# Kernel optimization log

Measured on AMD Instinct MI355X. Metric: run time of the kernel, lower is better.

Reference implementation:

```python
import jax, jax.numpy as jnp
import numpy as np

NUM_HEADS = 12
DIM = 768
NV = 4  # number of views
EPS = 1e-6


def _ln(x, g, b):
    m = x.mean(-1, keepdims=True)
    v = ((x - m) ** 2).mean(-1, keepdims=True)
    return (x - m) / jnp.sqrt(v + EPS) * g + b


def setup_inputs() -> dict:
    key = jax.random.key(0)
    ks = jax.random.split(key, 10)
    B, N, C, H = 4, 256, DIM, NUM_HEADS
    Hid = 4 * C
    s = 0.02
    return {
        'X': jax.random.normal(ks[0], (B * NV, N, C), jnp.float32),
        'norm1_g': jnp.ones((C,), jnp.float32),
        'norm1_b': jnp.zeros((C,), jnp.float32),
        'qkv_w': jax.random.normal(ks[1], (NV, 3 * C, C), jnp.float32) * s,
        'proj_w': jax.random.normal(ks[2], (NV, C, C), jnp.float32) * s,
        'proj_b': jnp.zeros((NV, C), jnp.float32),
        'norm2_g': jnp.ones((NV, C), jnp.float32),
        'norm2_b': jnp.zeros((NV, C), jnp.float32),
        'fc1_w': jax.random.normal(ks[3], (NV, Hid, C), jnp.float32) * s,
        'fc1_b': jnp.zeros((NV, Hid), jnp.float32),
        'fc2_w': jax.random.normal(ks[4], (NV, C, Hid), jnp.float32) * s,
        'fc2_b': jnp.zeros((NV, C), jnp.float32),
        'query': jax.random.normal(ks[5], (1, 1, C), jnp.float32),
        'mha_in_w': jax.random.normal(ks[6], (NV, 3 * C, C), jnp.float32) * s,
        'mha_in_b': jnp.zeros((NV, 3 * C), jnp.float32),
        'mha_out_w': jax.random.normal(ks[7], (NV, C, C), jnp.float32) * s,
        'mha_out_b': jnp.zeros((NV, C), jnp.float32),
    }


def reference(X, norm1_g, norm1_b, qkv_w, proj_w, proj_b, norm2_g, norm2_b,
              fc1_w, fc1_b, fc2_w, fc2_b, query, mha_in_w, mha_in_b,
              mha_out_w, mha_out_b):
    B4, N, C = X.shape
    B = B4 // NV
    H = NUM_HEADS
    hd = C // H
    scale = hd ** -0.5

    Xv = X.reshape(B, NV, N, C)
    Xn = _ln(Xv, norm1_g, norm1_b)

    # ---- FusionAttention: 4x4 pairwise cross attention between views ----
    qkv = jnp.einsum('bvnc,vdc->vbnd', Xn, qkv_w)              # [V,B,N,3C]
    qkv = qkv.reshape(NV, B, N, 3, H, hd).transpose(3, 0, 1, 4, 2, 5)  # [3,V,B,H,N,hd]
    q, k, v = qkv[0], qkv[1], qkv[2]
    scores = jnp.einsum('ibhnd,jbhmd->ijbhnm', q, k) * scale   # [V,V,B,H,N,N]
    attn = jax.nn.softmax(scores, axis=-1)
    ctx = jnp.einsum('ijbhnm,jbhmd->ijbhnd', attn, v)
    ctx = ctx.transpose(0, 1, 2, 4, 3, 5).reshape(NV, NV, B, N, C)
    # proj_i is affine, so mean over j of proj(x_j) == proj(mean_j x_j)
    ctx_mean = ctx.mean(axis=1)                                # [V,B,N,C]
    xa = jnp.einsum('vbnc,voc->vbno', ctx_mean, proj_w) + proj_b[:, None, None, :]

    x = xa * 2.0
    h = _ln(x, norm2_g[:, None, None, :], norm2_b[:, None, None, :])
    h1 = jax.nn.gelu(jnp.einsum('vbnc,vhc->vbnh', h, fc1_w) + fc1_b[:, None, None, :],
                     approximate=False)
    h2 = jnp.einsum('vbnh,vch->vbnc', h1, fc2_w) + fc2_b[:, None, None, :]
    x = x + h2                                                  # [V,B,N,C]

    # ---- CrossAttentionWithLearnableQuery (query identical for all T,B) ----
    wq, wk, wv = jnp.split(mha_in_w, 3, axis=1)                 # each [V,C,C]
    bq, bk, bv = jnp.split(mha_in_b, 3, axis=1)                 # each [V,C]
    q0 = query.reshape(C)
    qh = (jnp.einsum('c,vdc->vd', q0, wq) + bq).reshape(NV, H, hd)
    kh = (jnp.einsum('vbnc,vdc->vbnd', x, wk) + bk[:, None, None, :]).reshape(NV, B, N, H, hd)
    vh = (jnp.einsum('vbnc,vdc->vbnd', x, wv) + bv[:, None, None, :]).reshape(NV, B, N, H, hd)
    s2 = jnp.einsum('vhd,vbnhd->vbhn', qh, kh) * scale
    a2 = jax.nn.softmax(s2, axis=-1)
    c2 = jnp.einsum('vbhn,vbnhd->vbhd', a2, vh).reshape(NV, B, C)
    o = jnp.einsum('vbc,voc->vbo', c2, mha_out_w) + mha_out_b[:, None, :]  # [V,B,C]
    o = o.transpose(1, 0, 2).reshape(B, NV * C)                 # concat views
    # every query position produces identical output -> broadcast over T=N
    return jnp.broadcast_to(o[:, None, :], (B, N, NV * C))
```

## Files before the change

kernel.cpp:

```cpp
#include <hip/hip_runtime.h>
#include <math.h>

#define NVIEW 4
#define BATCH 4
#define NSEQ  256
#define CDIM  768
#define HEADS 12
#define HD    64

typedef __attribute__((ext_vector_type(8))) short   short8;
typedef __attribute__((ext_vector_type(8))) unsigned short ushort8;
typedef __attribute__((ext_vector_type(4))) float   float4v;

typedef const __attribute__((address_space(1))) void gas_t;
typedef       __attribute__((address_space(3))) void las_t;

__device__ __forceinline__ unsigned short f2b(float x)
{
    union { float f; unsigned u; } c; c.f = x;
    unsigned r = (c.u + 0x7FFFu + ((c.u >> 16) & 1u)) >> 16;
    return (unsigned short)r;
}

__global__ void conv_bf16(const float* __restrict__ src, unsigned short* __restrict__ dst, int n)
{
    int idx = (blockIdx.x * 256 + threadIdx.x) * 8;
    if (idx >= n) return;
    float4 a = *(const float4*)(src + idx);
    float4 b = *(const float4*)(src + idx + 4);
    ushort8 o;
    o[0] = f2b(a.x); o[1] = f2b(a.y); o[2] = f2b(a.z); o[3] = f2b(a.w);
    o[4] = f2b(b.x); o[5] = f2b(b.y); o[6] = f2b(b.z); o[7] = f2b(b.w);
    *(ushort8*)(dst + idx) = o;
}

__device__ __forceinline__ void block_ln_row_b(const float* __restrict__ xrow,
                                               const float* __restrict__ g,
                                               const float* __restrict__ b,
                                               unsigned short* __restrict__ orow)
{
    const int t = threadIdx.x;
    float x0 = xrow[t], x1 = xrow[t + 256], x2 = xrow[t + 512];
    float s  = x0 + x1 + x2;
    float s2 = x0 * x0 + x1 * x1 + x2 * x2;
    #pragma unroll
    for (int off = 32; off > 0; off >>= 1) {
        s  += __shfl_down(s, off);
        s2 += __shfl_down(s2, off);
    }
    __shared__ float w1[4], w2[4];
    if ((t & 63) == 0) { w1[t >> 6] = s; w2[t >> 6] = s2; }
    __syncthreads();
    float S  = w1[0] + w1[1] + w1[2] + w1[3];
    float S2 = w2[0] + w2[1] + w2[2] + w2[3];
    float mean = S * (1.0f / 768.0f);
    float var  = S2 * (1.0f / 768.0f) - mean * mean;
    float inv  = rsqrtf(var + 1e-6f);
    orow[t]       = f2b((x0 - mean) * inv * g[t]       + b[t]);
    orow[t + 256] = f2b((x1 - mean) * inv * g[t + 256] + b[t + 256]);
    orow[t + 512] = f2b((x2 - mean) * inv * g[t + 512] + b[t + 512]);
}

__global__ void ln1_kernel(const float* __restrict__ X, const float* __restrict__ g,
                           const float* __restrict__ b, unsigned short* __restrict__ Xn)
{
    int rid = blockIdx.x;
    int n  = rid & 255;
    int bv = rid >> 8;
    int bb = bv >> 2, v = bv & 3;
    const float* xrow = X + (long)rid * CDIM;
    unsigned short* orow = Xn + ((long)(v * 4 + bb) * 256 + n) * CDIM;
    block_ln_row_b(xrow, g, b, orow);
}

__global__ void ln2_kernel(const float* __restrict__ Xin, const float* __restrict__ g,
                           const float* __restrict__ b, unsigned short* __restrict__ Out)
{
    int rid = blockIdx.x;
    int v = rid >> 10;
    const float* xrow = Xin + (long)rid * CDIM;
    block_ln_row_b(xrow, g + v * CDIM, b + v * CDIM, Out + (long)rid * CDIM);
}

template <int EPI, int TM, typename OT>
__launch_bounds__(256, 2)
__global__ void gemm_bf16(const unsigned short* __restrict__ A,
                          const unsigned short* __restrict__ W,
                          const float* __restrict__ bias, const float* __restrict__ resid,
                          OT* __restrict__ out, int M, int N, int K,
                          long wStride, long wOff, int bStride, int bOff)
{
    const int v = blockIdx.z;
    const unsigned short* Av = A + (long)v * M * K;
    const unsigned short* Wv = W + v * wStride + wOff;

    __shared__ unsigned short As[TM * 64];
    __shared__ unsigned short Bs[128 * 64];

    const int tid  = threadIdx.x;
    const int lane = tid & 63;
    const int wave = tid >> 6;
    const int l15  = lane & 15;
    const int quad = lane >> 4;
    const int row0 = blockIdx.y * TM, col0 = blockIdx.x * 128;

    constexpr int MI = 4;
    constexpr int NI = (TM == 128) ? 4 : 2;
    const int mw = (TM == 128) ? (wave & 1) * 64 : 0;
    const int nw = (TM == 128) ? (wave >> 1) * 64 : wave * 32;

    float4v acc[MI][NI];
    #pragma unroll
    for (int i = 0; i < MI; ++i)
        #pragma unroll
        for (int j = 0; j < NI; ++j)
            acc[i][j] = (float4v){0.f, 0.f, 0.f, 0.f};

    const int lr8 = lane >> 3;
    const int p8  = lane & 7;

    for (int k0 = 0; k0 < K; k0 += 64) {
        __syncthreads();
        #pragma unroll
        for (int g = 0; g < TM / 32; ++g) {
            int G = wave * (TM / 32) + g;
            int r = G * 8 + lr8;
            int c = p8 ^ (r & 7);
            const unsigned short* sa = Av + (long)(row0 + r) * K + k0 + c * 8;
            __builtin_amdgcn_global_load_lds((gas_t*)sa, (las_t*)&As[G * 512], 16, 0, 0);
        }
        #pragma unroll
        for (int g = 0; g < 4; ++g) {
            int G = wave * 4 + g;
            int r = G * 8 + lr8;
            int c = p8 ^ (r & 7);
            const unsigned short* sw = Wv + (long)(col0 + r) * K + k0 + c * 8;
            __builtin_amdgcn_global_load_lds((gas_t*)sw, (las_t*)&Bs[G * 512], 16, 0, 0);
        }
        __syncthreads();

        #pragma unroll
        for (int ks = 0; ks < 2; ++ks) {
            short8 af[MI], bfr[NI];
            #pragma unroll
            for (int mi = 0; mi < MI; ++mi) {
                int m = mw + mi * 16 + l15;
                int p = (ks * 4 + quad) ^ (m & 7);
                af[mi] = *(const short8*)&As[m * 64 + p * 8];
            }
            #pragma unroll
            for (int ni = 0; ni < NI; ++ni) {
                int n = nw + ni * 16 + l15;
                int p = (ks * 4 + quad) ^ (n & 7);
                bfr[ni] = *(const short8*)&Bs[n * 64 + p * 8];
            }
            #pragma unroll
            for (int mi = 0; mi < MI; ++mi)
                #pragma unroll
                for (int ni = 0; ni < NI; ++ni)
                    acc[mi][ni] = __builtin_amdgcn_mfma_f32_16x16x32_bf16(af[mi], bfr[ni], acc[mi][ni], 0, 0, 0);
        }
    }

    #pragma unroll
    for (int mi = 0; mi < MI; ++mi) {
        #pragma unroll
        for (int ni = 0; ni < NI; ++ni) {
            int rowb = row0 + mw + mi * 16 + quad * 4;
            int col  = col0 + nw + ni * 16 + l15;
            float bval = 0.f;
            if (EPI >= 1) bval = bias[v * bStride + bOff + col];
            #pragma unroll
            for (int r = 0; r < 4; ++r) {
                float x = acc[mi][ni][r] + bval;
                long off = (long)v * M * N + (long)(rowb + r) * N + col;
                if constexpr (EPI == 2) {
                    x = 0.5f * x * (1.0f + erff(x * 0.70710678118654752f));
                } else if constexpr (EPI == 3) {
                    x += resid[off];
                } else if constexpr (EPI == 4) {
                    x *= 2.0f;
                }
                if constexpr (sizeof(OT) == 2) ((unsigned short*)out)[off] = f2b(x);
                else                           ((float*)out)[off] = x;
            }
        }
    }
}

__launch_bounds__(256, 2)
__global__ void fusion_attn_mfma(const unsigned short* __restrict__ QKV,
                                 unsigned short* __restrict__ ctx)
{
    const int qt = blockIdx.x;
    const int b  = blockIdx.y / HEADS;
    const int h  = blockIdx.y % HEADS;
    const int i  = blockIdx.z;
    const int tid  = threadIdx.x;
    const int lane = tid & 63;
    const int wave = tid >> 6;
    const int l15  = lane & 15;
    const int quad = lane >> 4;

    __shared__ unsigned short Qs[64 * 72];
    __shared__ unsigned short Ks[128 * 64];
    __shared__ unsigned short Ps[64 * 136];
    __shared__ unsigned short Vt[64 * 136];

    {
        int r = tid >> 2, p16 = (tid & 3) * 16;
        const unsigned short* src = QKV + ((long)((i * 4 + b) * 256 + qt * 64 + r)) * 2304 + h * 64 + p16;
        *(ushort8*)(&Qs[r * 72 + p16])     = *(const ushort8*)(src);
        *(ushort8*)(&Qs[r * 72 + p16 + 8]) = *(const ushort8*)(src + 8);
    }

    float4v acc_o[4];
    #pragma unroll
    for (int e = 0; e < 4; ++e) acc_o[e] = (float4v){0.f, 0.f, 0.f, 0.f};

    for (int j = 0; j < 4; ++j) {
        const unsigned short* Kb = QKV + ((long)((j * 4 + b) * 256)) * 2304 + 768 + h * 64;
        const unsigned short* Vb = Kb + 768;

        float4v sacc[16];
        #pragma unroll
        for (int t = 0; t < 16; ++t) sacc[t] = (float4v){0.f, 0.f, 0.f, 0.f};

        for (int half = 0; half < 2; ++half) {
            __syncthreads();
            #pragma unroll
            for (int g = 0; g < 4; ++g) {
                int R = wave * 32 + g * 8;
                int r = R + (lane >> 3);
                int p = lane & 7;
                int c = (p - (r & 7)) & 7;
                const unsigned short* src = Kb + (long)(half * 128 + r) * 2304 + c * 8;
                __builtin_amdgcn_global_load_lds((gas_t*)src, (las_t*)&Ks[R * 64], 16, 0, 0);
            }
            __syncthreads();
            #pragma unroll
            for (int ks = 0; ks < 2; ++ks) {
                int lcq = ks * 4 + quad;
                short8 qf = *(const short8*)&Qs[(wave * 16 + l15) * 72 + lcq * 8];
                #pragma unroll
                for (int nn = 0; nn < 8; ++nn) {
                    int n = nn * 16 + l15;
                    int p = (lcq + (n & 7)) & 7;
                    short8 kf = *(const short8*)&Ks[n * 64 + p * 8];
                    sacc[half * 8 + nn] =
                        __builtin_amdgcn_mfma_f32_16x16x32_bf16(qf, kf, sacc[half * 8 + nn], 0, 0, 0);
                }
            }
        }

        float rmax[4] = {-1e30f, -1e30f, -1e30f, -1e30f};
        #pragma unroll
        for (int t = 0; t < 16; ++t)
            #pragma unroll
            for (int r = 0; r < 4; ++r)
                rmax[r] = fmaxf(rmax[r], sacc[t][r] * 0.125f);
        #pragma unroll
        for (int off = 1; off < 16; off <<= 1)
            #pragma unroll
            for (int r = 0; r < 4; ++r)
                rmax[r] = fmaxf(rmax[r], __shfl_xor(rmax[r], off));
        float rsum[4] = {0.f, 0.f, 0.f, 0.f};
        #pragma unroll
        for (int t = 0; t < 16; ++t)
            #pragma unroll
            for (int r = 0; r < 4; ++r) {
                float e = __expf(sacc[t][r] * 0.125f - rmax[r]);
                sacc[t][r] = e;
                rsum[r] += e;
            }
        #pragma unroll
        for (int off = 1; off < 16; off <<= 1)
            #pragma unroll
            for (int r = 0; r < 4; ++r)
                rsum[r] += __shfl_xor(rsum[r], off);
        float invl[4];
        #pragma unroll
        for (int r = 0; r < 4; ++r) invl[r] = 1.0f / rsum[r];

        float4v pv[4];
        #pragma unroll
        for (int e = 0; e < 4; ++e) pv[e] = (float4v){0.f, 0.f, 0.f, 0.f};

        for (int half = 0; half < 2; ++half) {
            __syncthreads();
            #pragma unroll
            for (int nn = 0; nn < 8; ++nn)
                #pragma unroll
                for (int r = 0; r < 4; ++r)
                    Ps[(wave * 16 + quad * 4 + r) * 136 + nn * 16 + l15] = f2b(sacc[half * 8 + nn][r]);
            {
                int n = tid & 127;
                int c0 = (tid >> 7) * 4;
                #pragma unroll
                for (int cc = 0; cc < 4; ++cc) {
                    int c = c0 + cc;
                    ushort8 vv = *(const ushort8*)(Vb + (long)(half * 128 + n) * 2304 + c * 8);
                    #pragma unroll
                    for (int jj = 0; jj < 8; ++jj)
                        Vt[(c * 8 + jj) * 136 + n] = vv[jj];
                }
            }
            __syncthreads();
            #pragma unroll
            for (int ks = 0; ks < 4; ++ks) {
                int lc = ks * 4 + quad;
                short8 pf = *(const short8*)&Ps[(wave * 16 + l15) * 136 + lc * 8];
                #pragma unroll
                for (int et = 0; et < 4; ++et) {
                    short8 vf = *(const short8*)&Vt[(et * 16 + l15) * 136 + lc * 8];
                    pv[et] = __builtin_amdgcn_mfma_f32_16x16x32_bf16(pf, vf, pv[et], 0, 0, 0);
                }
            }
        }
        #pragma unroll
        for (int et = 0; et < 4; ++et)
            #pragma unroll
            for (int r = 0; r < 4; ++r)
                acc_o[et][r] += pv[et][r] * invl[r];
    }

    #pragma unroll
    for (int et = 0; et < 4; ++et)
        #pragma unroll
        for (int r = 0; r < 4; ++r) {
            int row = (i * 4 + b) * 256 + qt * 64 + wave * 16 + quad * 4 + r;
            int col = h * 64 + et * 16 + l15;
            ctx[(long)row * 768 + col] = f2b(acc_o[et][r] * 0.25f);
        }
}

__launch_bounds__(256, 4)
__global__ void qh_kernel(const float* __restrict__ query, const float* __restrict__ Win,
                          const float* __restrict__ Bin, float* __restrict__ QH)
{
    const int bi   = blockIdx.x;
    const int v    = bi / 192;
    const int dblk = bi - v * 192;
    const int t    = threadIdx.x;
    const int wave = t >> 6;
    const int lane = t & 63;
    const int d    = dblk * 4 + wave;

    __shared__ float qs[768];
    for (int idx = t; idx < 768; idx += 256) qs[idx] = query[idx];
    __syncthreads();

    const float* w = Win + ((long)v * 2304 + d) * 768;
    float acc = 0.f;
    #pragma unroll
    for (int k = 0; k < 3; ++k) {
        int c = k * 256 + lane * 4;
        float4 w4 = *(const float4*)(w + c);
        float4 q4 = *(const float4*)&qs[c];
        acc += w4.x * q4.x + w4.y * q4.y + w4.z * q4.z + w4.w * q4.w;
    }
    #pragma unroll
    for (int off = 32; off > 0; off >>= 1) acc += __shfl_down(acc, off);
    if (lane == 0)
        QH[v * 768 + d] = acc + Bin[(long)v * 2304 + d];
}

__launch_bounds__(256, 2)
__global__ void cross_attn(const float* __restrict__ KVH, const float* __restrict__ QH,
                           float* __restrict__ C2)
{
    const int h = blockIdx.x, b = blockIdx.y, v = blockIdx.z;
    const int t = threadIdx.x;
    __shared__ float qv[64];
    __shared__ float p[256];
    __shared__ float part[4][64];
    __shared__ float wred[4], wred2[4];

    if (t < 64) qv[t] = QH[(v * 12 + h) * 64 + t];
    __syncthreads();

    const float* krow = KVH + ((long)((v * 4 + b) * 256 + t)) * 1536 + h * 64;
    float s = 0.f;
    #pragma unroll
    for (int e = 0; e < 64; e += 4) {
        float4 k4 = *(const float4*)(krow + e);
        s += qv[e] * k4.x + qv[e + 1] * k4.y + qv[e + 2] * k4.z + qv[e + 3] * k4.w;
    }
    s *= 0.125f;
    float m4 = s;
    #pragma unroll
    for (int off = 32; off > 0; off >>= 1) m4 = fmaxf(m4, __shfl_down(m4, off));
    if ((t & 63) == 0) wred[t >> 6] = m4;
    __syncthreads();
    float rmax = fmaxf(fmaxf(wred[0], wred[1]), fmaxf(wred[2], wred[3]));
    float ev = __expf(s - rmax);
    p[t] = ev;
    float s4 = ev;
    #pragma unroll
    for (int off = 32; off > 0; off >>= 1) s4 += __shfl_down(s4, off);
    if ((t & 63) == 0) wred2[t >> 6] = s4;
    __syncthreads();
    float inv = 1.0f / (wred2[0] + wred2[1] + wred2[2] + wred2[3]);

    const int e = t & 63, ch = t >> 6;
    const float* vbase = KVH + ((long)((v * 4 + b) * 256)) * 1536 + 768 + h * 64 + e;
    float accv = 0.f;
    for (int m = ch * 64; m < ch * 64 + 64; ++m)
        accv += p[m] * vbase[(long)m * 1536];
    part[ch][e] = accv;
    __syncthreads();
    if (t < 64)
        C2[(v * 4 + b) * 768 + h * 64 + t] =
            (part[0][t] + part[1][t] + part[2][t] + part[3][t]) * inv;
}

__launch_bounds__(256, 4)
__global__ void out_matvec(const float* __restrict__ C2, const float* __restrict__ Wout,
                           const float* __restrict__ Bout, float* __restrict__ obc)
{
    const int bi   = blockIdx.x;
    const int v    = bi / 192;
    const int dblk = bi - v * 192;
    const int t    = threadIdx.x;
    const int wave = t >> 6;
    const int lane = t & 63;
    const int d    = dblk * 4 + wave;

    __shared__ float c2s[3072];
    #pragma unroll
    for (int idx = 0; idx < 3072; idx += 256) c2s[idx + t] = C2[v * 3072 + idx + t];
    __syncthreads();

    const float* w = Wout + ((long)v * 768 + d) * 768;
    float acc0 = 0.f, acc1 = 0.f, acc2 = 0.f, acc3 = 0.f;
    #pragma unroll
    for (int k = 0; k < 3; ++k) {
        int c = k * 256 + lane * 4;
        float4 w4 = *(const float4*)(w + c);
        float4 a0 = *(const float4*)&c2s[c];
        float4 a1 = *(const float4*)&c2s[768 + c];
        float4 a2 = *(const float4*)&c2s[1536 + c];
        float4 a3 = *(const float4*)&c2s[2304 + c];
        acc0 += w4.x * a0.x + w4.y * a0.y + w4.z * a0.z + w4.w * a0.w;
        acc1 += w4.x * a1.x + w4.y * a1.y + w4.z * a1.z + w4.w * a1.w;
        acc2 += w4.x * a2.x + w4.y * a2.y + w4.z * a2.z + w4.w * a2.w;
        acc3 += w4.x * a3.x + w4.y * a3.y + w4.z * a3.z + w4.w * a3.w;
    }
    #pragma unroll
    for (int off = 32; off > 0; off >>= 1) {
        acc0 += __shfl_down(acc0, off);
        acc1 += __shfl_down(acc1, off);
        acc2 += __shfl_down(acc2, off);
        acc3 += __shfl_down(acc3, off);
    }
    if (lane == 0) {
        float bb = Bout[v * 768 + d];
        obc[0 * 3072 + v * 768 + d] = acc0 + bb;
        obc[1 * 3072 + v * 768 + d] = acc1 + bb;
        obc[2 * 3072 + v * 768 + d] = acc2 + bb;
        obc[3 * 3072 + v * 768 + d] = acc3 + bb;
    }
}

__launch_bounds__(256, 4)
__global__ void out_bcast(const float* __restrict__ obc, float* __restrict__ out)
{
    const int b  = blockIdx.x >> 6;
    const int n0 = (blockIdx.x & 63) * 4;
    const int t  = threadIdx.x;
    const float4* src = (const float4*)(obc + (long)b * 3072);
    float4 v0 = src[t], v1 = src[t + 256], v2 = src[t + 512];
    float4* dst = (float4*)(out + ((long)(b * 256 + n0)) * 3072);
    #pragma unroll
    for (int r = 0; r < 4; ++r) {
        dst[r * 768 + t]       = v0;
        dst[r * 768 + t + 256] = v1;
        dst[r * 768 + t + 512] = v2;
    }
}

extern "C" void kernel_launch(void* const* d_in, const int* in_sizes, int n_in,
                              void* d_out, int out_size, void* d_ws, size_t ws_size,
                              hipStream_t stream)
{
    const float* X        = (const float*)d_in[0];
    const float* n1g      = (const float*)d_in[1];
    const float* n1b      = (const float*)d_in[2];
    const float* qkv_w    = (const float*)d_in[3];
    const float* proj_w   = (const float*)d_in[4];
    const float* proj_b   = (const float*)d_in[5];
    const float* n2g      = (const float*)d_in[6];
    const float* n2b      = (const float*)d_in[7];
    const float* fc1_w    = (const float*)d_in[8];
    const float* fc1_b    = (const float*)d_in[9];
    const float* fc2_w    = (const float*)d_in[10];
    const float* fc2_b    = (const float*)d_in[11];
    const float* query    = (const float*)d_in[12];
    const float* mha_in_w = (const float*)d_in[13];
    const float* mha_in_b = (const float*)d_in[14];
    const float* mha_out_w= (const float*)d_in[15];
    const float* mha_out_b= (const float*)d_in[16];
    float* out = (float*)d_out;

    char* wsb = (char*)d_ws;
    unsigned short* wbuf = (unsigned short*)wsb;
    unsigned short* rgA  = (unsigned short*)(wsb + 18874368);
    char*           rgB  = wsb + 25165824;
    float*          xbuf = (float*)(wsb + 50331648);
    float*          qh   = (float*)(wsb + 62914560);
    float*          c2   = (float*)(wsb + 62926848);
    float*          obc  = (float*)(wsb + 62976000);

    unsigned short* QKV = (unsigned short*)rgB;
    unsigned short* H1  = (unsigned short*)rgB;
    float*          KVH = (float*)rgB;

    conv_bf16<<<3456, 256, 0, stream>>>(qkv_w, wbuf, 7077888);
    ln1_kernel<<<4096, 256, 0, stream>>>(X, n1g, n1b, rgA);
    gemm_bf16<0, 128, unsigned short><<<dim3(18, 8, 4), 256, 0, stream>>>(
        rgA, wbuf, nullptr, nullptr, QKV, 1024, 2304, 768, 2304L * 768, 0, 0, 0);
    fusion_attn_mfma<<<dim3(4, 48, 4), 256, 0, stream>>>(QKV, rgA);
    conv_bf16<<<1152, 256, 0, stream>>>(proj_w, wbuf, 2359296);
    gemm_bf16<4, 64, float><<<dim3(6, 16, 4), 256, 0, stream>>>(
        rgA, wbuf, proj_b, nullptr, xbuf, 1024, 768, 768, 768L * 768, 0, 768, 0);
    ln2_kernel<<<4096, 256, 0, stream>>>(xbuf, n2g, n2b, rgA);
    conv_bf16<<<4608, 256, 0, stream>>>(fc1_w, wbuf, 9437184);
    gemm_bf16<2, 128, unsigned short><<<dim3(24, 8, 4), 256, 0, stream>>>(
        rgA, wbuf, fc1_b, nullptr, H1, 1024, 3072, 768, 3072L * 768, 0, 3072, 0);
    conv_bf16<<<4608, 256, 0, stream>>>(fc2_w, wbuf, 9437184);
    gemm_bf16<3, 64, unsigned short><<<dim3(6, 16, 4), 256, 0, stream>>>(
        H1, wbuf, fc2_b, xbuf, rgA, 1024, 768, 3072, 768L * 3072, 0, 768, 0);
    conv_bf16<<<3456, 256, 0, stream>>>(mha_in_w, wbuf, 7077888);
    gemm_bf16<1, 64, float><<<dim3(12, 16, 4), 256, 0, stream>>>(
        rgA, wbuf, mha_in_b, nullptr, KVH, 1024, 1536, 768, 2304L * 768, 768L * 768, 2304, 768);
    qh_kernel<<<768, 256, 0, stream>>>(query, mha_in_w, mha_in_b, qh);
    cross_attn<<<dim3(12, 4, 4), 256, 0, stream>>>(KVH, qh, c2);
    out_matvec<<<768, 256, 0, stream>>>(c2, mha_out_w, mha_out_b, obc);
    out_bcast<<<256, 256, 0, stream>>>(obc, out);
}
```

Before: 447.1 us.

## Write V transposed from QKV GEMM epilogue and stream it directly in attention

The QKV GEMM epilogue now writes the V slice in a per-head transposed layout to a separate buffer, so the attention kernel reads V fragments straight from global memory instead of transposing V through shared memory. The QK MFMA operands are swapped so each lane holds a full score row, which turns the softmax reductions into two cross-half shuffles and lets P be stored to LDS as packed 64-bit writes. Removing the Vt shared buffer frees LDS, and the occupancy hint is raised from 2 to 3 blocks. In exchange, the GEMM epilogue does scattered 2-byte stores for the V columns, and V is read from global memory inside the inner MFMA loop.

```diff
diff --git a/kernel.cpp b/kernel.cpp
--- a/kernel.cpp
+++ b/kernel.cpp
@@ -87,7 +87,8 @@
 __global__ void gemm_bf16(const unsigned short* __restrict__ A,
                           const unsigned short* __restrict__ W,
                           const float* __restrict__ bias, const float* __restrict__ resid,
-                          OT* __restrict__ out, int M, int N, int K,
+                          OT* __restrict__ out, unsigned short* __restrict__ vt,
+                          int M, int N, int K,
                           long wStride, long wOff, int bStride, int bOff)
 {
     const int v = blockIdx.z;
@@ -169,7 +170,7 @@
             int rowb = row0 + mw + mi * 16 + quad * 4;
             int col  = col0 + nw + ni * 16 + l15;
             float bval = 0.f;
-            if (EPI >= 1) bval = bias[v * bStride + bOff + col];
+            if (EPI >= 1 && EPI <= 4) bval = bias[v * bStride + bOff + col];
             #pragma unroll
             for (int r = 0; r < 4; ++r) {
                 float x = acc[mi][ni][r] + bval;
@@ -181,15 +182,29 @@
                 } else if constexpr (EPI == 4) {
                     x *= 2.0f;
                 }
-                if constexpr (sizeof(OT) == 2) ((unsigned short*)out)[off] = f2b(x);
-                else                           ((float*)out)[off] = x;
-            }
-        }
-    }
-}
-
-__launch_bounds__(256, 2)
+                if constexpr (EPI == 7) {
+                    if (col0 < 1536) {
+                        ((unsigned short*)out)[off] = f2b(x);
+                    } else {
+                        int cc  = col - 1536;
+                        int hh  = cc >> 6, ee = cc & 63;
+                        int row = rowb + r;
+                        int bb2 = row >> 8, nn2 = row & 255;
+                        vt[((long)((v * 4 + bb2) * 12 + hh)) * 16384 + ee * 256 + nn2] = f2b(x);
+                    }
+                } else if constexpr (sizeof(OT) == 2) {
+                    ((unsigned short*)out)[off] = f2b(x);
+                } else {
+                    ((float*)out)[off] = x;
+                }
+            }
+        }
+    }
+}
+
+__launch_bounds__(256, 3)
 __global__ void fusion_attn_mfma(const unsigned short* __restrict__ QKV,
+                                 const unsigned short* __restrict__ VT,
                                  unsigned short* __restrict__ ctx)
 {
     const int qt = blockIdx.x;
@@ -205,7 +220,6 @@
     __shared__ unsigned short Qs[64 * 72];
     __shared__ unsigned short Ks[128 * 64];
     __shared__ unsigned short Ps[64 * 136];
-    __shared__ unsigned short Vt[64 * 136];
 
     {
         int r = tid >> 2, p16 = (tid & 3) * 16;
@@ -219,8 +233,8 @@
     for (int e = 0; e < 4; ++e) acc_o[e] = (float4v){0.f, 0.f, 0.f, 0.f};
 
     for (int j = 0; j < 4; ++j) {
-        const unsigned short* Kb = QKV + ((long)((j * 4 + b) * 256)) * 2304 + 768 + h * 64;
-        const unsigned short* Vb = Kb + 768;
+        const unsigned short* Kb  = QKV + ((long)((j * 4 + b) * 256)) * 2304 + 768 + h * 64;
+        const unsigned short* VTb = VT + ((long)((j * 4 + b) * 12 + h)) * 16384;
 
         float4v sacc[16];
         #pragma unroll
@@ -248,80 +262,64 @@
                     int p = (lcq + (n & 7)) & 7;
                     short8 kf = *(const short8*)&Ks[n * 64 + p * 8];
                     sacc[half * 8 + nn] =
-                        __builtin_amdgcn_mfma_f32_16x16x32_bf16(qf, kf, sacc[half * 8 + nn], 0, 0, 0);
+                        __builtin_amdgcn_mfma_f32_16x16x32_bf16(kf, qf, sacc[half * 8 + nn], 0, 0, 0);
                 }
             }
         }
 
-        float rmax[4] = {-1e30f, -1e30f, -1e30f, -1e30f};
+        float rmax = -1e30f;
         #pragma unroll
         for (int t = 0; t < 16; ++t)
             #pragma unroll
             for (int r = 0; r < 4; ++r)
-                rmax[r] = fmaxf(rmax[r], sacc[t][r] * 0.125f);
-        #pragma unroll
-        for (int off = 1; off < 16; off <<= 1)
-            #pragma unroll
-            for (int r = 0; r < 4; ++r)
-                rmax[r] = fmaxf(rmax[r], __shfl_xor(rmax[r], off));
-        float rsum[4] = {0.f, 0.f, 0.f, 0.f};
+                rmax = fmaxf(rmax, sacc[t][r] * 0.125f);
+        rmax = fmaxf(rmax, __shfl_xor(rmax, 16));
+        rmax = fmaxf(rmax, __shfl_xor(rmax, 32));
+        float rsum = 0.f;
         #pragma unroll
         for (int t = 0; t < 16; ++t)
             #pragma unroll
             for (int r = 0; r < 4; ++r) {
-                float e = __expf(sacc[t][r] * 0.125f - rmax[r]);
+                float e = __expf(sacc[t][r] * 0.125f - rmax);
                 sacc[t][r] = e;
-                rsum[r] += e;
-            }
-        #pragma unroll
-        for (int off = 1; off < 16; off <<= 1)
-            #pragma unroll
-            for (int r = 0; r < 4; ++r)
-                rsum[r] += __shfl_xor(rsum[r], off);
-        float invl[4];
-        #pragma unroll
-        for (int r = 0; r < 4; ++r) invl[r] = 1.0f / rsum[r];
+                rsum += e;
+            }
+        rsum += __shfl_xor(rsum, 16);
+        rsum += __shfl_xor(rsum, 32);
+        float invl = 1.0f / rsum;
+        float invq[4];
+        #pragma unroll
+        for (int r = 0; r < 4; ++r) invq[r] = __shfl(invl, quad * 4 + r);
 
         float4v pv[4];
         #pragma unroll
         for (int e = 0; e < 4; ++e) pv[e] = (float4v){0.f, 0.f, 0.f, 0.f};
 
         for (int half = 0; half < 2; ++half) {
+            #pragma unroll
+            for (int nn = 0; nn < 8; ++nn) {
+                uint2 pk;
+                pk.x = (unsigned)f2b(sacc[half * 8 + nn][0]) | ((unsigned)f2b(sacc[half * 8 + nn][1]) << 16);
+                pk.y = (unsigned)f2b(sacc[half * 8 + nn][2]) | ((unsigned)f2b(sacc[half * 8 + nn][3]) << 16);
+                *(uint2*)&Ps[(wave * 16 + l15) * 136 + nn * 16 + quad * 4] = pk;
+            }
             __syncthreads();
             #pragma unroll
-            for (int nn = 0; nn < 8; ++nn)
-                #pragma unroll
-                for (int r = 0; r < 4; ++r)
-                    Ps[(wave * 16 + quad * 4 + r) * 136 + nn * 16 + l15] = f2b(sacc[half * 8 + nn][r]);
-            {
-                int n = tid & 127;
-                int c0 = (tid >> 7) * 4;
-                #pragma unroll
-                for (int cc = 0; cc < 4; ++cc) {
-                    int c = c0 + cc;
-                    ushort8 vv = *(const ushort8*)(Vb + (long)(half * 128 + n) * 2304 + c * 8);
-                    #pragma unroll
-                    for (int jj = 0; jj < 8; ++jj)
-                        Vt[(c * 8 + jj) * 136 + n] = vv[jj];
-                }
-            }
-            __syncthreads();
-            #pragma unroll
             for (int ks = 0; ks < 4; ++ks) {
-                int lc = ks * 4 + quad;
-                short8 pf = *(const short8*)&Ps[(wave * 16 + l15) * 136 + lc * 8];
+                short8 pf = *(const short8*)&Ps[(wave * 16 + l15) * 136 + ks * 32 + quad * 8];
                 #pragma unroll
                 for (int et = 0; et < 4; ++et) {
-                    short8 vf = *(const short8*)&Vt[(et * 16 + l15) * 136 + lc * 8];
+                    short8 vf = *(const short8*)(VTb + (long)(et * 16 + l15) * 256 + half * 128 + ks * 32 + quad * 8);
                     pv[et] = __builtin_amdgcn_mfma_f32_16x16x32_bf16(pf, vf, pv[et], 0, 0, 0);
                 }
             }
+            __syncthreads();
         }
         #pragma unroll
         for (int et = 0; et < 4; ++et)
             #pragma unroll
             for (int r = 0; r < 4; ++r)
-                acc_o[et][r] += pv[et][r] * invl[r];
+                acc_o[et][r] += pv[et][r] * invq[r];
     }
 
     #pragma unroll
@@ -512,27 +510,28 @@
     float*          obc  = (float*)(wsb + 62976000);
 
     unsigned short* QKV = (unsigned short*)rgB;
+    unsigned short* VTb = (unsigned short*)(wsb + 44040192);
     unsigned short* H1  = (unsigned short*)rgB;
     float*          KVH = (float*)rgB;
 
     conv_bf16<<<3456, 256, 0, stream>>>(qkv_w, wbuf, 7077888);
     ln1_kernel<<<4096, 256, 0, stream>>>(X, n1g, n1b, rgA);
-    gemm_bf16<0, 128, unsigned short><<<dim3(18, 8, 4), 256, 0, stream>>>(
-        rgA, wbuf, nullptr, nullptr, QKV, 1024, 2304, 768, 2304L * 768, 0, 0, 0);
-    fusion_attn_mfma<<<dim3(4, 48, 4), 256, 0, stream>>>(QKV, rgA);
+    gemm_bf16<7, 128, unsigned short><<<dim3(18, 8, 4), 256, 0, stream>>>(
+        rgA, wbuf, nullptr, nullptr, QKV, VTb, 1024, 2304, 768, 2304L * 768, 0, 0, 0);
+    fusion_attn_mfma<<<dim3(4, 48, 4), 256, 0, stream>>>(QKV, VTb, rgA);
     conv_bf16<<<1152, 256, 0, stream>>>(proj_w, wbuf, 2359296);
     gemm_bf16<4, 64, float><<<dim3(6, 16, 4), 256, 0, stream>>>(
-        rgA, wbuf, proj_b, nullptr, xbuf, 1024, 768, 768, 768L * 768, 0, 768, 0);
+        rgA, wbuf, proj_b, nullptr, xbuf, nullptr, 1024, 768, 768, 768L * 768, 0, 768, 0);
     ln2_kernel<<<4096, 256, 0, stream>>>(xbuf, n2g, n2b, rgA);
     conv_bf16<<<4608, 256, 0, stream>>>(fc1_w, wbuf, 9437184);
     gemm_bf16<2, 128, unsigned short><<<dim3(24, 8, 4), 256, 0, stream>>>(
-        rgA, wbuf, fc1_b, nullptr, H1, 1024, 3072, 768, 3072L * 768, 0, 3072, 0);
+        rgA, wbuf, fc1_b, nullptr, H1, nullptr, 1024, 3072, 768, 3072L * 768, 0, 3072, 0);
     conv_bf16<<<4608, 256, 0, stream>>>(fc2_w, wbuf, 9437184);
     gemm_bf16<3, 64, unsigned short><<<dim3(6, 16, 4), 256, 0, stream>>>(
-        H1, wbuf, fc2_b, xbuf, rgA, 1024, 768, 3072, 768L * 3072, 0, 768, 0);
+        H1, wbuf, fc2_b, xbuf, rgA, nullptr, 1024, 768, 3072, 768L * 3072, 0, 768, 0);
     conv_bf16<<<3456, 256, 0, stream>>>(mha_in_w, wbuf, 7077888);
     gemm_bf16<1, 64, float><<<dim3(12, 16, 4), 256, 0, stream>>>(
-        rgA, wbuf, mha_in_b, nullptr, KVH, 1024, 1536, 768, 2304L * 768, 768L * 768, 2304, 768);
+        rgA, wbuf, mha_in_b, nullptr, KVH, nullptr, 1024, 1536, 768, 2304L * 768, 768L * 768, 2304, 768);
     qh_kernel<<<768, 256, 0, stream>>>(query, mha_in_w, mha_in_b, qh);
     cross_attn<<<dim3(12, 4, 4), 256, 0, stream>>>(KVH, qh, c2);
     out_matvec<<<768, 256, 0, stream>>>(c2, mha_out_w, mha_out_b, obc);
```

Measured after the change: 465.8 us. +4.2%, slower.
